# Performance work log

Hardware: AMD Instinct MI355X
Metric: run time of the kernel (lower is better)

The kernel has to match this reference:

```python
import jax, jax.numpy as jnp
import numpy as np

B, T, NF, T2V, GH, NH, GRUH = 128, 256, 17, 16, 32, 4, 128


def _t2v(t, w0, b0, W, Bp):
    # t: [...] -> [..., T2V] = [linear term, sin periodic terms]
    lin = t[..., None] * w0 + b0
    per = jnp.sin(t[..., None] * W + Bp)
    return jnp.concatenate([lin, per], axis=-1)


def _gat(h, adj, W, a_src, a_dst, residual):
    # h: [N, F, Din], W: [Din, H, O], a_*: [H, O]; batched multi-head GAT over N graphs
    p = jnp.einsum('nfd,dho->nfho', h, W)
    es = jnp.einsum('nfho,ho->nhf', p, a_src)
    ed = jnp.einsum('nfho,ho->nhf', p, a_dst)
    e = jax.nn.leaky_relu(es[:, :, :, None] + ed[:, :, None, :], 0.2)  # [N,H,F,F]
    e = jnp.where(adj[None, None] > 0, e, jnp.float32(-1e9))
    a = jax.nn.softmax(e, axis=-1)
    out = jnp.einsum('nhij,njho->niho', a, p).reshape(h.shape[0], h.shape[1], -1)
    if residual:
        out = out + h
    return jax.nn.elu(out)


def _gru_dir(x, wih, whh, bih, bhh, reverse):
    # PyTorch GRU gate order [r, z, n]; x: [B,T,D] -> (outputs [B,T,H], h_final [B,H])
    gx = jnp.einsum('btd,gd->btg', x, wih) + bih
    if reverse:
        gx = gx[:, ::-1]
    H = whh.shape[1]

    def step(h, gxt):
        gh = h @ whh.T + bhh
        r = jax.nn.sigmoid(gxt[:, :H] + gh[:, :H])
        z = jax.nn.sigmoid(gxt[:, H:2 * H] + gh[:, H:2 * H])
        n = jnp.tanh(gxt[:, 2 * H:] + r * gh[:, 2 * H:])
        h2 = (1.0 - z) * n + z * h
        return h2, h2

    h0 = jnp.zeros((x.shape[0], H), x.dtype)
    hT, ys = jax.lax.scan(step, h0, jnp.swapaxes(gx, 0, 1))
    ys = jnp.swapaxes(ys, 0, 1)
    if reverse:
        ys = ys[:, ::-1]
    return ys, hT


def setup_inputs() -> dict:
    key = jax.random.key(0)
    ks = iter(jax.random.split(key, 64))

    def nrm(shape, fan):
        return jax.random.normal(next(ks), shape, jnp.float32) / np.float32(np.sqrt(fan))

    X = jax.random.normal(next(ks), (B, T, NF), jnp.float32)
    mask = (jax.random.uniform(next(ks), (B, T, NF)) > 0.3).astype(jnp.float32)
    delta = jax.random.uniform(next(ks), (B, T, NF), jnp.float32) * 10.0
    times = jnp.broadcast_to(jnp.arange(T, dtype=jnp.float32)[None], (B, T)) + jax.random.uniform(next(ks), (B, T), jnp.float32)
    adj = jnp.ones((NF, NF), jnp.float32) - jnp.eye(NF, dtype=jnp.float32)

    D0 = 2 + 2 * T2V  # node_in_dim = 34
    GO = GH * NH      # gat_out_dim = 128
    inp = dict(X=X, mask=mask, delta=delta, times=times, adj=adj,
               aw0=nrm((1,), 1), ab0=nrm((1,), 1), aW=nrm((T2V - 1,), 1), aB=nrm((T2V - 1,), 1),
               dw0=nrm((1,), 1), db0=nrm((1,), 1), dW=nrm((T2V - 1,), 1), dB=nrm((T2V - 1,), 1),
               gW0=nrm((D0, NH, GH), D0), gas0=nrm((NH, GH), GH), gad0=nrm((NH, GH), GH),
               gW1=nrm((GO, NH, GH), GO), gas1=nrm((NH, GH), GH), gad1=nrm((NH, GH), GH))
    for name, ind in [('g0f', GO), ('g0b', GO), ('g1f', 2 * GRUH), ('g1b', 2 * GRUH)]:
        inp[name + '_wih'] = nrm((3 * GRUH, ind), ind)
        inp[name + '_whh'] = nrm((3 * GRUH, GRUH), GRUH)
        inp[name + '_bih'] = jnp.zeros((3 * GRUH,), jnp.float32)
        inp[name + '_bhh'] = jnp.zeros((3 * GRUH,), jnp.float32)
    pd = 2 * GRUH
    inp.update(mh_w1=nrm((64, pd), pd), mh_b1=jnp.zeros((64,), jnp.float32),
               mh_w2=nrm((1, 64), 64), mh_b2=jnp.zeros((1,), jnp.float32),
               ch_w1=nrm((64, pd), pd), ch_b1=jnp.zeros((64,), jnp.float32),
               ch_w2=nrm((1, 64), 64), ch_b2=jnp.zeros((1,), jnp.float32))
    return inp


def reference(X, mask, delta, times, adj, aw0, ab0, aW, aB, dw0, db0, dW, dB,
              gW0, gas0, gad0, gW1, gas1, gad1,
              g0f_wih, g0f_whh, g0f_bih, g0f_bhh, g0b_wih, g0b_whh, g0b_bih, g0b_bhh,
              g1f_wih, g1f_whh, g1f_bih, g1f_bhh, g1b_wih, g1b_whh, g1b_bih, g1b_bhh,
              mh_w1, mh_b1, mh_w2, mh_b2, ch_w1, ch_b1, ch_w2, ch_b2):
    Bx, Tx, F = X.shape
    # node features: [x, mask, time2vec(t), time2vec(delta)] -> [B,T,F,34]
    t_emb = _t2v(times, aw0, ab0, aW, aB)
    t_emb = jnp.broadcast_to(t_emb[:, :, None, :], (Bx, Tx, F, T2V))
    d_emb = _t2v(delta, dw0, db0, dW, dB)
    nf = jnp.concatenate([X[..., None], mask[..., None], t_emb, d_emb], axis=-1)
    # batched GAT over all B*T graphs at once (replaces the Python bt-loop)
    h = nf.reshape(Bx * Tx, F, nf.shape[-1])
    h = _gat(h, adj, gW0, gas0, gad0, False)
    h = _gat(h, adj, gW1, gas1, gad1, True)
    z = h.mean(axis=1).reshape(Bx, Tx, NH * GH)
    # bidirectional 2-layer GRU
    yf, _ = _gru_dir(z, g0f_wih, g0f_whh, g0f_bih, g0f_bhh, False)
    yb, _ = _gru_dir(z, g0b_wih, g0b_whh, g0b_bih, g0b_bhh, True)
    y = jnp.concatenate([yf, yb], axis=-1)
    yf1, hf1 = _gru_dir(y, g1f_wih, g1f_whh, g1f_bih, g1f_bhh, False)
    yb1, hb1 = _gru_dir(y, g1b_wih, g1b_whh, g1b_bih, g1b_bhh, True)
    gru_out = jnp.concatenate([yf1, yb1], axis=-1)
    patient_emb = jnp.concatenate([hf1, hb1], axis=-1)
    m = jax.nn.relu(patient_emb @ mh_w1.T + mh_b1) @ mh_w2.T + mh_b2
    risk = jax.nn.relu(patient_emb @ ch_w1.T + ch_b1) @ ch_w2.T + ch_b2
    return (m, jax.nn.sigmoid(m), risk, patient_emb, gru_out)
```

## Files before the change

### kernel.cpp

```cpp
#include <hip/hip_runtime.h>
#include <hip/hip_bf16.h>
#include <math.h>

#define NFE 17
#define T2V 16
#define D0C 34
#define BB 128
#define TT 256
#define HH 128
#define PSTR 132
#define ASTR 136
#define KSTR 40
#define ESTR 40
#define EHSTR 680

typedef __hip_bfloat16 bf16;
__device__ __forceinline__ float b2f(bf16 x) { return __bfloat162float(x); }

typedef __attribute__((ext_vector_type(8))) __bf16 bfrag;
typedef __attribute__((ext_vector_type(4))) float  ffrag;
typedef __attribute__((ext_vector_type(4))) __bf16 bf4;

__device__ __forceinline__ float elu_fast(float v)  { return v > 0.f ? v : __expf(v) - 1.f; }
__device__ __forceinline__ float sigm_fast(float x) { return __fdividef(1.f, 1.f + __expf(-x)); }
__device__ __forceinline__ float tanh_fast(float x) {
  return __fdividef(2.f, 1.f + __expf(-2.f*x)) - 1.f;
}

__device__ __bf16 g_W0h[8192],  g_W0l[8192];
__device__ __bf16 g_W1h[16384], g_W1l[16384];

__global__ __launch_bounds__(256) void prep_w(const float* __restrict__ W0,
                                              const float* __restrict__ W1) {
  const int tid = blockIdx.x*256 + threadIdx.x;
  if (tid < 16384) {
    const int j = tid & 7, lane = (tid >> 3) & 63, ks = (tid >> 9) & 3, nt = tid >> 11;
    const int n = nt*16 + (lane & 15), k = ks*32 + (lane >> 4)*8 + j;
    const float v = W1[k*128 + n];
    const __bf16 hi = (__bf16)v;
    g_W1h[tid] = hi;
    g_W1l[tid] = (__bf16)(v - (float)hi);
  }
  if (tid < 8192) {
    const int j = tid & 7, lane = (tid >> 3) & 63, ks = (tid >> 9) & 1, nt = tid >> 10;
    const int n = nt*16 + (lane & 15), k = ks*32 + (lane >> 4)*8 + j;
    const float v = (k < D0C) ? W0[k*128 + n] : 0.f;
    const __bf16 hi = (__bf16)v;
    g_W0h[tid] = hi;
    g_W0l[tid] = (__bf16)(v - (float)hi);
  }
}

template<int KSTEPS>
__device__ __forceinline__ void gat_proj_mfma(const __bf16* s_ah, const __bf16* s_al,
                                              const __bf16* __restrict__ Wth,
                                              const __bf16* __restrict__ Wtl,
                                              float* s_p, __bf16* s_pth, __bf16* s_ptl,
                                              int tid)
{
  const int lane = tid & 63, wv = tid >> 6;
  const int mn = lane & 15, q = lane >> 4;
  ffrag acc[2][2] = {};
  #pragma unroll
  for (int ks = 0; ks < KSTEPS; ++ks) {
    const bfrag ah0 = *(const bfrag*)&s_ah[(     mn)*ASTR + ks*32 + q*8];
    const bfrag al0 = *(const bfrag*)&s_al[(     mn)*ASTR + ks*32 + q*8];
    const bfrag ah1 = *(const bfrag*)&s_ah[(16 + mn)*ASTR + ks*32 + q*8];
    const bfrag al1 = *(const bfrag*)&s_al[(16 + mn)*ASTR + ks*32 + q*8];
    #pragma unroll
    for (int nt = 0; nt < 2; ++nt) {
      const int fi = (((wv*2 + nt)*KSTEPS + ks)*64 + lane)*8;
      const bfrag bh = *(const bfrag*)&Wth[fi];
      const bfrag bl = *(const bfrag*)&Wtl[fi];
      acc[0][nt] = __builtin_amdgcn_mfma_f32_16x16x32_bf16(al0, bh, acc[0][nt], 0,0,0);
      acc[0][nt] = __builtin_amdgcn_mfma_f32_16x16x32_bf16(ah0, bl, acc[0][nt], 0,0,0);
      acc[0][nt] = __builtin_amdgcn_mfma_f32_16x16x32_bf16(ah0, bh, acc[0][nt], 0,0,0);
      acc[1][nt] = __builtin_amdgcn_mfma_f32_16x16x32_bf16(al1, bh, acc[1][nt], 0,0,0);
      acc[1][nt] = __builtin_amdgcn_mfma_f32_16x16x32_bf16(ah1, bl, acc[1][nt], 0,0,0);
      acc[1][nt] = __builtin_amdgcn_mfma_f32_16x16x32_bf16(ah1, bh, acc[1][nt], 0,0,0);
    }
  }
  const int n0 = wv*32;
  #pragma unroll
  for (int nt = 0; nt < 2; ++nt) {
    const int col = n0 + nt*16 + mn;
    __bf16 hbuf[4], lbuf[4];
    #pragma unroll
    for (int i = 0; i < 4; ++i) {
      const float v = acc[0][nt][i];
      s_p[(q*4 + i)*PSTR + col] = v;
      const __bf16 hi = (__bf16)v;
      hbuf[i] = hi;
      lbuf[i] = (__bf16)(v - (float)hi);
    }
    *(bf4*)&s_pth[col*KSTR + q*4] = *(bf4*)hbuf;
    *(bf4*)&s_ptl[col*KSTR + q*4] = *(bf4*)lbuf;
    if (q == 0) {
      const float v = acc[1][nt][0];
      s_p[16*PSTR + col] = v;
      const __bf16 hi = (__bf16)v;
      s_pth[col*KSTR + 16] = hi;
      s_ptl[col*KSTR + 16] = (__bf16)(v - (float)hi);
    }
  }
}

__device__ __forceinline__ void gat_scoresm(const float* s_p,
                                            const float* __restrict__ asrc,
                                            const float* __restrict__ adst,
                                            const float* s_adj,
                                            __bf16* s_Eh, __bf16* s_El, int tid) {
  const int lane = tid & 63, h = tid >> 6;
  const int f = lane & 31;
  float sc = 0.f;
  if (f < NFE) {
    const float* av = (lane < 32) ? asrc : adst;
    #pragma unroll
    for (int o = 0; o < 32; o += 4) {
      const float4 p4 = *(const float4*)&s_p[f*PSTR + h*32 + o];
      const float4 a4 = *(const float4*)&av[h*32 + o];
      sc = fmaf(p4.x, a4.x, sc); sc = fmaf(p4.y, a4.y, sc);
      sc = fmaf(p4.z, a4.z, sc); sc = fmaf(p4.w, a4.w, sc);
    }
  }
  float ed[NFE];
  #pragma unroll
  for (int j = 0; j < NFE; ++j) ed[j] = __shfl(sc, 32 + j);
  if (lane < NFE) {
    const int i = lane;
    const float esv = sc;
    float row[NFE]; float mx = -1e30f;
    #pragma unroll
    for (int j = 0; j < NFE; ++j) {
      float v = -1.0e9f;
      if (s_adj[i*NFE + j] > 0.f) {
        const float e = esv + ed[j];
        v = (e > 0.f) ? e : 0.2f*e;
      }
      row[j] = v; mx = fmaxf(mx, v);
    }
    float sum = 0.f;
    #pragma unroll
    for (int j = 0; j < NFE; ++j) { row[j] = __expf(row[j] - mx); sum += row[j]; }
    const float inv = __fdividef(1.f, sum);
    __bf16 hrow[32], lrow[32];
    #pragma unroll
    for (int j = 0; j < 32; ++j) {
      const float v = (j < NFE) ? row[j]*inv : 0.f;
      const __bf16 hi = (__bf16)v;
      hrow[j] = hi;
      lrow[j] = (__bf16)(v - (float)hi);
    }
    #pragma unroll
    for (int w = 0; w < 4; ++w) {
      *(bfrag*)&s_Eh[h*EHSTR + i*ESTR + w*8] = *(bfrag*)&hrow[w*8];
      *(bfrag*)&s_El[h*EHSTR + i*ESTR + w*8] = *(bfrag*)&lrow[w*8];
    }
  }
}

__device__ __forceinline__ void gat_out_core(const __bf16* s_Eh, const __bf16* s_El,
                                             const __bf16* s_pth, const __bf16* s_ptl,
                                             int wv, int mn, int q, ffrag acc[2][2]) {
  const bfrag eh0 = *(const bfrag*)&s_Eh[wv*EHSTR + mn*ESTR + q*8];
  const bfrag el0 = *(const bfrag*)&s_El[wv*EHSTR + mn*ESTR + q*8];
  const bfrag eh1 = *(const bfrag*)&s_Eh[wv*EHSTR + (16+mn)*ESTR + q*8];
  const bfrag el1 = *(const bfrag*)&s_El[wv*EHSTR + (16+mn)*ESTR + q*8];
  #pragma unroll
  for (int nt = 0; nt < 2; ++nt) {
    const int nrow = wv*32 + nt*16 + mn;
    const bfrag ph = *(const bfrag*)&s_pth[nrow*KSTR + q*8];
    const bfrag pl = *(const bfrag*)&s_ptl[nrow*KSTR + q*8];
    acc[0][nt] = __builtin_amdgcn_mfma_f32_16x16x32_bf16(el0, ph, acc[0][nt], 0,0,0);
    acc[0][nt] = __builtin_amdgcn_mfma_f32_16x16x32_bf16(eh0, pl, acc[0][nt], 0,0,0);
    acc[0][nt] = __builtin_amdgcn_mfma_f32_16x16x32_bf16(eh0, ph, acc[0][nt], 0,0,0);
    acc[1][nt] = __builtin_amdgcn_mfma_f32_16x16x32_bf16(el1, ph, acc[1][nt], 0,0,0);
    acc[1][nt] = __builtin_amdgcn_mfma_f32_16x16x32_bf16(eh1, pl, acc[1][nt], 0,0,0);
    acc[1][nt] = __builtin_amdgcn_mfma_f32_16x16x32_bf16(eh1, ph, acc[1][nt], 0,0,0);
  }
}

__device__ __forceinline__ void gat_out0(const __bf16* s_Eh, const __bf16* s_El,
                                         const __bf16* s_pth, const __bf16* s_ptl,
                                         __bf16* s_ah, __bf16* s_al, int tid) {
  const int lane = tid & 63, wv = tid >> 6;
  const int mn = lane & 15, q = lane >> 4;
  ffrag acc[2][2] = {};
  gat_out_core(s_Eh, s_El, s_pth, s_ptl, wv, mn, q, acc);
  #pragma unroll
  for (int nt = 0; nt < 2; ++nt) {
    const int c = wv*32 + nt*16 + mn;
    #pragma unroll
    for (int i = 0; i < 4; ++i) {
      const float v = elu_fast(acc[0][nt][i]);
      const __bf16 hi = (__bf16)v;
      s_ah[(q*4+i)*ASTR + c] = hi;
      s_al[(q*4+i)*ASTR + c] = (__bf16)(v - (float)hi);
    }
    if (q == 0) {
      const float v = elu_fast(acc[1][nt][0]);
      const __bf16 hi = (__bf16)v;
      s_ah[16*ASTR + c] = hi;
      s_al[16*ASTR + c] = (__bf16)(v - (float)hi);
    }
  }
}

__device__ __forceinline__ void gat_out1(const __bf16* s_Eh, const __bf16* s_El,
                                         const __bf16* s_pth, const __bf16* s_ptl,
                                         const __bf16* s_ah, const __bf16* s_al,
                                         float* __restrict__ zrow, int tid) {
  const int lane = tid & 63, wv = tid >> 6;
  const int mn = lane & 15, q = lane >> 4;
  ffrag acc[2][2] = {};
  gat_out_core(s_Eh, s_El, s_pth, s_ptl, wv, mn, q, acc);
  #pragma unroll
  for (int nt = 0; nt < 2; ++nt) {
    const int c = wv*32 + nt*16 + mn;
    float sum = 0.f;
    #pragma unroll
    for (int i = 0; i < 4; ++i) {
      const int r = q*4 + i;
      const float res = (float)s_ah[r*ASTR + c] + (float)s_al[r*ASTR + c];
      sum += elu_fast(acc[0][nt][i] + res);
    }
    sum += __shfl_xor(sum, 16);
    sum += __shfl_xor(sum, 32);
    if (q == 0) {
      const float res = (float)s_ah[16*ASTR + c] + (float)s_al[16*ASTR + c];
      sum += elu_fast(acc[1][nt][0] + res);
      zrow[c] = sum * (1.0f/17.0f);
    }
  }
}

__global__ __launch_bounds__(256) void gat_fused(
    const float* __restrict__ X,  const float* __restrict__ Mk,
    const float* __restrict__ Dl, const float* __restrict__ Tm,
    const float* __restrict__ Adj,
    const float* __restrict__ aw0, const float* __restrict__ ab0,
    const float* __restrict__ aW,  const float* __restrict__ aB,
    const float* __restrict__ dw0, const float* __restrict__ db0,
    const float* __restrict__ dW,  const float* __restrict__ dB,
    const float* __restrict__ as0, const float* __restrict__ ad0,
    const float* __restrict__ as1, const float* __restrict__ ad1,
    float* __restrict__ zslot)
{
  __shared__ __align__(16) unsigned char smem[50816];
  __bf16* s_ah  = (__bf16*)(smem);
  __bf16* s_al  = (__bf16*)(smem + 4624);
  float*  s_p   = (float*)(smem + 9248);
  __bf16* s_Eh  = (__bf16*)(smem + 18224);
  __bf16* s_El  = (__bf16*)(smem + 23664);
  __bf16* s_pth = (__bf16*)(smem + 29104);
  __bf16* s_ptl = (__bf16*)(smem + 39344);
  float*  s_t   = (float*)(smem + 49584);
  float*  s_adj = (float*)(smem + 49648);
  const int n = blockIdx.x;
  const int tid = threadIdx.x;

  {
    const float4 z4 = {0.f, 0.f, 0.f, 0.f};
    float4* zp = (float4*)(smem + 29104);
    for (int i = tid; i < 1280; i += 256) zp[i] = z4;
  }
  const float tv = Tm[n];
  if (tid < T2V) {
    s_t[tid] = (tid == 0) ? fmaf(tv, aw0[0], ab0[0])
                          : __sinf(fmaf(tv, aW[tid-1], aB[tid-1]));
  }
  for (int idx = tid; idx < NFE*NFE; idx += 256) s_adj[idx] = Adj[idx];
  __syncthreads();
  for (int idx = tid; idx < NFE*64; idx += 256) {
    const int f = idx >> 6, c = idx & 63;
    float v = 0.f;
    if (c == 0)            v = X [(size_t)n*NFE + f];
    else if (c == 1)       v = Mk[(size_t)n*NFE + f];
    else if (c < 2 + T2V)  v = s_t[c-2];
    else if (c < D0C) {
      const float dd = Dl[(size_t)n*NFE + f];
      const int j = c - (2 + T2V);
      v = (j == 0) ? fmaf(dd, dw0[0], db0[0])
                   : __sinf(fmaf(dd, dW[j-1], dB[j-1]));
    }
    const __bf16 hi = (__bf16)v;
    s_ah[f*ASTR + c] = hi;
    s_al[f*ASTR + c] = (__bf16)(v - (float)hi);
  }
  __syncthreads();
  gat_proj_mfma<2>(s_ah, s_al, g_W0h, g_W0l, s_p, s_pth, s_ptl, tid); __syncthreads();
  gat_scoresm(s_p, as0, ad0, s_adj, s_Eh, s_El, tid);                 __syncthreads();
  gat_out0(s_Eh, s_El, s_pth, s_ptl, s_ah, s_al, tid);                __syncthreads();
  gat_proj_mfma<4>(s_ah, s_al, g_W1h, g_W1l, s_p, s_pth, s_ptl, tid); __syncthreads();
  gat_scoresm(s_p, as1, ad1, s_adj, s_Eh, s_El, tid);                 __syncthreads();
  gat_out1(s_Eh, s_El, s_pth, s_ptl, s_ah, s_al,
           zslot + (size_t)n*256 + 128, tid);
}

__global__ __launch_bounds__(256) void gemm_xw_mfma(
    const float* __restrict__ A, int lda,
    const float* __restrict__ Wf, const float* __restrict__ biasf,
    bf16* __restrict__ Cf,
    const float* __restrict__ Wb, const float* __restrict__ biasb,
    bf16* __restrict__ Cb, int K)
{
  const float* W    = blockIdx.z ? Wb : Wf;
  const float* bias = blockIdx.z ? biasb : biasf;
  bf16*        C    = blockIdx.z ? Cb : Cf;
  __shared__ __bf16 Ah[64][40];
  __shared__ __bf16 Al[64][40];
  __shared__ __bf16 Wh[64][40];
  __shared__ __bf16 Wl[64][40];
  const int tid = threadIdx.x;
  const int bm0 = blockIdx.x * 64;
  const int bn0 = blockIdx.y * 64;
  const int lane = tid & 63, wv = tid >> 6;
  const int mn = lane & 15, q = lane >> 4;
  const int sr = tid >> 2, sk = (tid & 3) * 8;
  ffrag acc[4] = {};
  for (int kk = 0; kk < K; kk += 32) {
    {
      float av[8];
      *(float4*)&av[0] = *(const float4*)&A[(size_t)(bm0 + sr)*lda + kk + sk];
      *(float4*)&av[4] = *(const float4*)&A[(size_t)(bm0 + sr)*lda + kk + sk + 4];
      __bf16 th[8], tl[8];
      #pragma unroll
      for (int i = 0; i < 8; ++i) {
        const __bf16 hi = (__bf16)av[i];
        th[i] = hi;
        tl[i] = (__bf16)(av[i] - (float)hi);
      }
      *(bfrag*)&Ah[sr][sk] = *(bfrag*)th;
      *(bfrag*)&Al[sr][sk] = *(bfrag*)tl;
      float wv8[8];
      *(float4*)&wv8[0] = *(const float4*)&W[(size_t)(bn0 + sr)*K + kk + sk];
      *(float4*)&wv8[4] = *(const float4*)&W[(size_t)(bn0 + sr)*K + kk + sk + 4];
      __bf16 wh8[8], wl8[8];
      #pragma unroll
      for (int i = 0; i < 8; ++i) {
        const __bf16 hi = (__bf16)wv8[i];
        wh8[i] = hi;
        wl8[i] = (__bf16)(wv8[i] - (float)hi);
      }
      *(bfrag*)&Wh[sr][sk] = *(bfrag*)wh8;
      *(bfrag*)&Wl[sr][sk] = *(bfrag*)wl8;
    }
    __syncthreads();
    const bfrag afh = *(const bfrag*)&Ah[16*wv + mn][q*8];
    const bfrag afl = *(const bfrag*)&Al[16*wv + mn][q*8];
    #pragma unroll
    for (int t = 0; t < 4; ++t) {
      const bfrag bwh = *(const bfrag*)&Wh[16*t + mn][q*8];
      const bfrag bwl = *(const bfrag*)&Wl[16*t + mn][q*8];
      acc[t] = __builtin_amdgcn_mfma_f32_16x16x32_bf16(afl, bwh, acc[t], 0, 0, 0);
      acc[t] = __builtin_amdgcn_mfma_f32_16x16x32_bf16(afh, bwl, acc[t], 0, 0, 0);
      acc[t] = __builtin_amdgcn_mfma_f32_16x16x32_bf16(afh, bwh, acc[t], 0, 0, 0);
    }
    __syncthreads();
  }
  #pragma unroll
  for (int t = 0; t < 4; ++t) {
    const int col = bn0 + 16*t + mn;
    const float bv = bias[col];
    #pragma unroll
    for (int i = 0; i < 4; ++i) {
      const int row = bm0 + 16*wv + q*4 + i;
      C[(size_t)row*384 + col] = __float2bfloat16(acc[t][i] + bv);
    }
  }
}

__global__ __launch_bounds__(384, 1) void gru_rec(
    const bf16* __restrict__ gxf,
    const bf16* __restrict__ gxb,
    const float* __restrict__ whh_f, const float* __restrict__ whh_b,
    const float* __restrict__ bhh_f, const float* __restrict__ bhh_b,
    float* __restrict__ ys,
    float* __restrict__ hfin)
{
  const int blk = blockIdx.x;
  const int dir = blk >> 7;
  const int b   = blk & 127;
  const int g   = threadIdx.x;
  const float* whh = dir ? whh_b : whh_f;
  const float* bhh = dir ? bhh_b : bhh_f;
  const bf16* gx   = (dir ? gxb : gxf) + (size_t)b*TT*384;
  __shared__ __align__(16) float s_h[HH];
  __shared__ float s_gh[3*HH];
  __shared__ float s_gx[3*HH];
  float4 w[HH/4];
  #pragma unroll
  for (int d4 = 0; d4 < HH/4; ++d4)
    w[d4] = *(const float4*)&whh[(size_t)g*HH + 4*d4];
  const float bh = bhh[g];
  float hreg = 0.f;
  if (g < HH) s_h[g] = 0.f;
  __syncthreads();
  for (int s = 0; s < TT; ++s) {
    const int t = dir ? (TT-1-s) : s;
    const float gxv = b2f(gx[(size_t)t*384 + g]);
    float acc = bh;
    const float4* h4 = (const float4*)s_h;
    #pragma unroll
    for (int d4 = 0; d4 < HH/4; ++d4) {
      const float4 hv = h4[d4];
      acc = fmaf(hv.x, w[d4].x, acc);
      acc = fmaf(hv.y, w[d4].y, acc);
      acc = fmaf(hv.z, w[d4].z, acc);
      acc = fmaf(hv.w, w[d4].w, acc);
    }
    s_gh[g] = acc;
    s_gx[g] = gxv;
    __syncthreads();
    if (g < HH) {
      const float r  = sigm_fast(s_gx[g]    + s_gh[g]);
      const float zg = sigm_fast(s_gx[HH+g] + s_gh[HH+g]);
      const float nn = tanh_fast(s_gx[2*HH+g] + r*s_gh[2*HH+g]);
      hreg = (1.f - zg)*nn + zg*hreg;
      s_h[g] = hreg;
      ys[((size_t)b*TT + t)*256 + dir*HH + g] = hreg;
    }
    __syncthreads();
  }
  if (g < HH && hfin) hfin[(size_t)b*256 + dir*HH + g] = hreg;
}

__global__ __launch_bounds__(64) void heads_k(
    const float* __restrict__ pemb,
    const float* __restrict__ mw1, const float* __restrict__ mb1,
    const float* __restrict__ mw2, const float* __restrict__ mb2,
    const float* __restrict__ cw1, const float* __restrict__ cb1,
    const float* __restrict__ cw2, const float* __restrict__ cb2,
    float* __restrict__ out)
{
  const int b = blockIdx.x, tid = threadIdx.x;
  __shared__ float sh[64];
  const float* pe = pemb + (size_t)b*256;
  float acc = mb1[tid];
  for (int d = 0; d < 256; ++d) acc = fmaf(pe[d], mw1[(size_t)tid*256 + d], acc);
  sh[tid] = fmaxf(acc, 0.f) * mw2[tid];
  __syncthreads();
  if (tid == 0) {
    float s = mb2[0];
    for (int i = 0; i < 64; ++i) s += sh[i];
    out[b]       = s;
    out[128 + b] = 1.f/(1.f + expf(-s));
  }
  __syncthreads();
  acc = cb1[tid];
  for (int d = 0; d < 256; ++d) acc = fmaf(pe[d], cw1[(size_t)tid*256 + d], acc);
  sh[tid] = fmaxf(acc, 0.f) * cw2[tid];
  __syncthreads();
  if (tid == 0) {
    float s = cb2[0];
    for (int i = 0; i < 64; ++i) s += sh[i];
    out[256 + b] = s;
  }
}

extern "C" void kernel_launch(void* const* d_in, const int* in_sizes, int n_in,
                              void* d_out, int out_size, void* d_ws, size_t ws_size,
                              hipStream_t stream) {
  const float* X    = (const float*)d_in[0];
  const float* Mk   = (const float*)d_in[1];
  const float* Dl   = (const float*)d_in[2];
  const float* Tm   = (const float*)d_in[3];
  const float* Adj  = (const float*)d_in[4];
  const float* aw0  = (const float*)d_in[5];
  const float* ab0  = (const float*)d_in[6];
  const float* aWt  = (const float*)d_in[7];
  const float* aBt  = (const float*)d_in[8];
  const float* dw0  = (const float*)d_in[9];
  const float* db0  = (const float*)d_in[10];
  const float* dWt  = (const float*)d_in[11];
  const float* dBt  = (const float*)d_in[12];
  const float* gW0  = (const float*)d_in[13];
  const float* gas0 = (const float*)d_in[14];
  const float* gad0 = (const float*)d_in[15];
  const float* gW1  = (const float*)d_in[16];
  const float* gas1 = (const float*)d_in[17];
  const float* gad1 = (const float*)d_in[18];
  const float* g0f_wih = (const float*)d_in[19];
  const float* g0f_whh = (const float*)d_in[20];
  const float* g0f_bih = (const float*)d_in[21];
  const float* g0f_bhh = (const float*)d_in[22];
  const float* g0b_wih = (const float*)d_in[23];
  const float* g0b_whh = (const float*)d_in[24];
  const float* g0b_bih = (const float*)d_in[25];
  const float* g0b_bhh = (const float*)d_in[26];
  const float* g1f_wih = (const float*)d_in[27];
  const float* g1f_whh = (const float*)d_in[28];
  const float* g1f_bih = (const float*)d_in[29];
  const float* g1f_bhh = (const float*)d_in[30];
  const float* g1b_wih = (const float*)d_in[31];
  const float* g1b_whh = (const float*)d_in[32];
  const float* g1b_bih = (const float*)d_in[33];
  const float* g1b_bhh = (const float*)d_in[34];
  const float* mh_w1 = (const float*)d_in[35];
  const float* mh_b1 = (const float*)d_in[36];
  const float* mh_w2 = (const float*)d_in[37];
  const float* mh_b2 = (const float*)d_in[38];
  const float* ch_w1 = (const float*)d_in[39];
  const float* ch_b1 = (const float*)d_in[40];
  const float* ch_w2 = (const float*)d_in[41];
  const float* ch_b2 = (const float*)d_in[42];

  bf16* gxA = (bf16*)d_ws;
  bf16* gxB = gxA + 12582912;

  float* out  = (float*)d_out;
  float* pemb = out + 384;
  float* slot = out + 384 + 32768;

  prep_w<<<64, 256, 0, stream>>>(gW0, gW1);

  gat_fused<<<dim3(BB*TT), dim3(256), 0, stream>>>(
      X, Mk, Dl, Tm, Adj, aw0, ab0, aWt, aBt, dw0, db0, dWt, dBt,
      gas0, gad0, gas1, gad1, slot);

  dim3 ggrid(32768/64, 384/64, 2);
  gemm_xw_mfma<<<ggrid, 256, 0, stream>>>(slot + 128, 256,
      g0f_wih, g0f_bih, gxA, g0b_wih, g0b_bih, gxB, 128);
  gru_rec<<<256, 384, 0, stream>>>(gxA, gxB, g0f_whh, g0b_whh, g0f_bhh, g0b_bhh,
                                   slot, nullptr);
  gemm_xw_mfma<<<ggrid, 256, 0, stream>>>(slot, 256,
      g1f_wih, g1f_bih, gxA, g1b_wih, g1b_bih, gxB, 256);
  gru_rec<<<256, 384, 0, stream>>>(gxA, gxB, g1f_whh, g1b_whh, g1f_bhh, g1b_bhh,
                                   slot, pemb);

  heads_k<<<128, 64, 0, stream>>>(pemb, mh_w1, mh_b1, mh_w2, mh_b2,
                                  ch_w1, ch_b1, ch_w2, ch_b2, out);
}
```

Before: 1.202 ms.

## Split GRU recurrence dot-product over two thread halves and drop fp32 GAT projection buffer

The GRU recurrent kernel now runs 768 threads per block, each pair of threads splitting the 128-long hidden dot product into two 64-wide halves. Partial sums are combined through a new shared buffer before the gate math. This halves per-thread serial FMA work and register-held weights on the latency-bound sequential loop, at the cost of more threads per barrier. Separately, the GAT kernel no longer writes an fp32 copy of the projection. Attention scores are computed from the transposed bf16 hi/lo split buffers instead, which cuts shared memory per block and may allow more resident blocks.

```diff
diff --git a/kernel.cpp b/kernel.cpp
--- a/kernel.cpp
+++ b/kernel.cpp
@@ -8,7 +8,6 @@
 #define BB 128
 #define TT 256
 #define HH 128
-#define PSTR 132
 #define ASTR 136
 #define KSTR 40
 #define ESTR 40
@@ -55,7 +54,7 @@
 __device__ __forceinline__ void gat_proj_mfma(const __bf16* s_ah, const __bf16* s_al,
                                               const __bf16* __restrict__ Wth,
                                               const __bf16* __restrict__ Wtl,
-                                              float* s_p, __bf16* s_pth, __bf16* s_ptl,
+                                              __bf16* s_pth, __bf16* s_ptl,
                                               int tid)
 {
   const int lane = tid & 63, wv = tid >> 6;
@@ -88,7 +87,6 @@
     #pragma unroll
     for (int i = 0; i < 4; ++i) {
       const float v = acc[0][nt][i];
-      s_p[(q*4 + i)*PSTR + col] = v;
       const __bf16 hi = (__bf16)v;
       hbuf[i] = hi;
       lbuf[i] = (__bf16)(v - (float)hi);
@@ -97,7 +95,6 @@
     *(bf4*)&s_ptl[col*KSTR + q*4] = *(bf4*)lbuf;
     if (q == 0) {
       const float v = acc[1][nt][0];
-      s_p[16*PSTR + col] = v;
       const __bf16 hi = (__bf16)v;
       s_pth[col*KSTR + 16] = hi;
       s_ptl[col*KSTR + 16] = (__bf16)(v - (float)hi);
@@ -105,7 +102,7 @@
   }
 }
 
-__device__ __forceinline__ void gat_scoresm(const float* s_p,
+__device__ __forceinline__ void gat_scoresm(const __bf16* s_pth, const __bf16* s_ptl,
                                             const float* __restrict__ asrc,
                                             const float* __restrict__ adst,
                                             const float* s_adj,
@@ -115,12 +112,11 @@
   float sc = 0.f;
   if (f < NFE) {
     const float* av = (lane < 32) ? asrc : adst;
-    #pragma unroll
-    for (int o = 0; o < 32; o += 4) {
-      const float4 p4 = *(const float4*)&s_p[f*PSTR + h*32 + o];
-      const float4 a4 = *(const float4*)&av[h*32 + o];
-      sc = fmaf(p4.x, a4.x, sc); sc = fmaf(p4.y, a4.y, sc);
-      sc = fmaf(p4.z, a4.z, sc); sc = fmaf(p4.w, a4.w, sc);
+    const int base = h*32*KSTR + f;
+    #pragma unroll
+    for (int o = 0; o < 32; ++o) {
+      const float p = (float)s_pth[base + o*KSTR] + (float)s_ptl[base + o*KSTR];
+      sc = fmaf(p, av[h*32 + o], sc);
     }
   }
   float ed[NFE];
@@ -246,22 +242,21 @@
     const float* __restrict__ as1, const float* __restrict__ ad1,
     float* __restrict__ zslot)
 {
-  __shared__ __align__(16) unsigned char smem[50816];
+  __shared__ __align__(16) unsigned char smem[41828];
   __bf16* s_ah  = (__bf16*)(smem);
   __bf16* s_al  = (__bf16*)(smem + 4624);
-  float*  s_p   = (float*)(smem + 9248);
-  __bf16* s_Eh  = (__bf16*)(smem + 18224);
-  __bf16* s_El  = (__bf16*)(smem + 23664);
-  __bf16* s_pth = (__bf16*)(smem + 29104);
-  __bf16* s_ptl = (__bf16*)(smem + 39344);
-  float*  s_t   = (float*)(smem + 49584);
-  float*  s_adj = (float*)(smem + 49648);
+  __bf16* s_Eh  = (__bf16*)(smem + 9248);
+  __bf16* s_El  = (__bf16*)(smem + 14688);
+  __bf16* s_pth = (__bf16*)(smem + 20128);
+  __bf16* s_ptl = (__bf16*)(smem + 30368);
+  float*  s_t   = (float*)(smem + 40608);
+  float*  s_adj = (float*)(smem + 40672);
   const int n = blockIdx.x;
   const int tid = threadIdx.x;
 
   {
     const float4 z4 = {0.f, 0.f, 0.f, 0.f};
-    float4* zp = (float4*)(smem + 29104);
+    float4* zp = (float4*)(smem + 20128);
     for (int i = tid; i < 1280; i += 256) zp[i] = z4;
   }
   const float tv = Tm[n];
@@ -288,11 +283,11 @@
     s_al[f*ASTR + c] = (__bf16)(v - (float)hi);
   }
   __syncthreads();
-  gat_proj_mfma<2>(s_ah, s_al, g_W0h, g_W0l, s_p, s_pth, s_ptl, tid); __syncthreads();
-  gat_scoresm(s_p, as0, ad0, s_adj, s_Eh, s_El, tid);                 __syncthreads();
-  gat_out0(s_Eh, s_El, s_pth, s_ptl, s_ah, s_al, tid);                __syncthreads();
-  gat_proj_mfma<4>(s_ah, s_al, g_W1h, g_W1l, s_p, s_pth, s_ptl, tid); __syncthreads();
-  gat_scoresm(s_p, as1, ad1, s_adj, s_Eh, s_El, tid);                 __syncthreads();
+  gat_proj_mfma<2>(s_ah, s_al, g_W0h, g_W0l, s_pth, s_ptl, tid);     __syncthreads();
+  gat_scoresm(s_pth, s_ptl, as0, ad0, s_adj, s_Eh, s_El, tid);       __syncthreads();
+  gat_out0(s_Eh, s_El, s_pth, s_ptl, s_ah, s_al, tid);               __syncthreads();
+  gat_proj_mfma<4>(s_ah, s_al, g_W1h, g_W1l, s_pth, s_ptl, tid);     __syncthreads();
+  gat_scoresm(s_pth, s_ptl, as1, ad1, s_adj, s_Eh, s_El, tid);       __syncthreads();
   gat_out1(s_Eh, s_El, s_pth, s_ptl, s_ah, s_al,
            zslot + (size_t)n*256 + 128, tid);
 }
@@ -370,7 +365,7 @@
   }
 }
 
-__global__ __launch_bounds__(384, 1) void gru_rec(
+__global__ __launch_bounds__(768, 1) void gru_rec(
     const bf16* __restrict__ gxf,
     const bf16* __restrict__ gxb,
     const float* __restrict__ whh_f, const float* __restrict__ whh_b,
@@ -382,47 +377,50 @@
   const int dir = blk >> 7;
   const int b   = blk & 127;
   const int g   = threadIdx.x;
+  const int p   = threadIdx.y;
   const float* whh = dir ? whh_b : whh_f;
   const float* bhh = dir ? bhh_b : bhh_f;
   const bf16* gx   = (dir ? gxb : gxf) + (size_t)b*TT*384;
   __shared__ __align__(16) float s_h[HH];
-  __shared__ float s_gh[3*HH];
-  __shared__ float s_gx[3*HH];
-  float4 w[HH/4];
-  #pragma unroll
-  for (int d4 = 0; d4 < HH/4; ++d4)
-    w[d4] = *(const float4*)&whh[(size_t)g*HH + 4*d4];
-  const float bh = bhh[g];
+  __shared__ float s_gh  [3*HH];
+  __shared__ float s_part[3*HH];
+  __shared__ float s_gx  [3*HH];
+  float4 w[HH/8];
+  #pragma unroll
+  for (int d4 = 0; d4 < HH/8; ++d4)
+    w[d4] = *(const float4*)&whh[(size_t)g*HH + p*64 + 4*d4];
+  const float bh = p ? 0.f : bhh[g];
   float hreg = 0.f;
-  if (g < HH) s_h[g] = 0.f;
+  if (p == 0 && g < HH) s_h[g] = 0.f;
   __syncthreads();
   for (int s = 0; s < TT; ++s) {
     const int t = dir ? (TT-1-s) : s;
-    const float gxv = b2f(gx[(size_t)t*384 + g]);
+    float gxv = 0.f;
+    if (p == 0) gxv = b2f(gx[(size_t)t*384 + g]);
     float acc = bh;
-    const float4* h4 = (const float4*)s_h;
-    #pragma unroll
-    for (int d4 = 0; d4 < HH/4; ++d4) {
+    const float4* h4 = (const float4*)&s_h[p*64];
+    #pragma unroll
+    for (int d4 = 0; d4 < HH/8; ++d4) {
       const float4 hv = h4[d4];
       acc = fmaf(hv.x, w[d4].x, acc);
       acc = fmaf(hv.y, w[d4].y, acc);
       acc = fmaf(hv.z, w[d4].z, acc);
       acc = fmaf(hv.w, w[d4].w, acc);
     }
-    s_gh[g] = acc;
-    s_gx[g] = gxv;
+    if (p == 0) { s_gh[g] = acc; s_gx[g] = gxv; }
+    else        { s_part[g] = acc; }
     __syncthreads();
-    if (g < HH) {
-      const float r  = sigm_fast(s_gx[g]    + s_gh[g]);
-      const float zg = sigm_fast(s_gx[HH+g] + s_gh[HH+g]);
-      const float nn = tanh_fast(s_gx[2*HH+g] + r*s_gh[2*HH+g]);
+    if (p == 0 && g < HH) {
+      const float r  = sigm_fast(s_gx[g]      + s_gh[g]      + s_part[g]);
+      const float zg = sigm_fast(s_gx[HH+g]   + s_gh[HH+g]   + s_part[HH+g]);
+      const float nn = tanh_fast(s_gx[2*HH+g] + r*(s_gh[2*HH+g] + s_part[2*HH+g]));
       hreg = (1.f - zg)*nn + zg*hreg;
       s_h[g] = hreg;
       ys[((size_t)b*TT + t)*256 + dir*HH + g] = hreg;
     }
     __syncthreads();
   }
-  if (g < HH && hfin) hfin[(size_t)b*256 + dir*HH + g] = hreg;
+  if (p == 0 && g < HH && hfin) hfin[(size_t)b*256 + dir*HH + g] = hreg;
 }
 
 __global__ __launch_bounds__(64) void heads_k(
@@ -521,12 +519,12 @@
   dim3 ggrid(32768/64, 384/64, 2);
   gemm_xw_mfma<<<ggrid, 256, 0, stream>>>(slot + 128, 256,
       g0f_wih, g0f_bih, gxA, g0b_wih, g0b_bih, gxB, 128);
-  gru_rec<<<256, 384, 0, stream>>>(gxA, gxB, g0f_whh, g0b_whh, g0f_bhh, g0b_bhh,
-                                   slot, nullptr);
+  gru_rec<<<256, dim3(384, 2), 0, stream>>>(gxA, gxB, g0f_whh, g0b_whh,
+                                            g0f_bhh, g0b_bhh, slot, nullptr);
   gemm_xw_mfma<<<ggrid, 256, 0, stream>>>(slot, 256,
       g1f_wih, g1f_bih, gxA, g1b_wih, g1b_bih, gxB, 256);
-  gru_rec<<<256, 384, 0, stream>>>(gxA, gxB, g1f_whh, g1b_whh, g1f_bhh, g1b_bhh,
-                                   slot, pemb);
+  gru_rec<<<256, dim3(384, 2), 0, stream>>>(gxA, gxB, g1f_whh, g1b_whh,
+                                            g1f_bhh, g1b_bhh, slot, pemb);
 
   heads_k<<<128, 64, 0, stream>>>(pemb, mh_w1, mh_b1, mh_w2, mh_b2,
                                   ch_w1, ch_b1, ch_w2, ch_b2, out);
```

Result: no change. 1.224 ms (+1.8%).
